# Kernel optimization log

Hardware: AMD Instinct MI355X
Metric: run time of the kernel (lower is better)

The kernel has to match this reference:

```python
import jax, jax.numpy as jnp
import numpy as np

# SemiConv2d with semifield_type='MaxMin':
#   out[n,oc,i,j] = max_{ic,kh,kw} min(x_pad[n,ic,i+kh,j+kw], kernel[oc,ic,kh,kw])
# stride=1, 'same' padding with -inf (identity of max).

def setup_inputs() -> dict:
    key = jax.random.key(0)
    kx, kk = jax.random.split(key)
    x = jax.random.normal(kx, (8, 32, 96, 96), dtype=jnp.float32)
    kernel = jax.random.normal(kk, (32, 32, 3, 3), dtype=jnp.float32)
    return {"x": x, "kernel": kernel}


def reference(x, kernel):
    N, IC, H, W = x.shape
    OC, IC2, KH, KW = kernel.shape
    assert IC == IC2
    # same padding for k=3, stride=1 (left=top=1, right=bottom=1)
    p = KH - 1
    top = left = p // 2
    bot = right = p - top
    xp = jnp.pad(x, ((0, 0), (0, 0), (top, bot), (left, right)),
                 constant_values=-jnp.inf)
    out = None
    # small fixed loop over kernel taps (KH*KW = 9); vectorized over N, OC, IC, H, W
    for kh in range(KH):
        for kw in range(KW):
            win = xp[:, :, kh:kh + H, kw:kw + W]           # [N, IC, H, W]
            k_tap = kernel[:, :, kh, kw]                   # [OC, IC]
            # min over values, max over input channels -> [N, OC, H, W]
            v = jnp.max(jnp.minimum(win[:, None], k_tap[None, :, :, None, None]), axis=2)
            out = v if out is None else jnp.maximum(out, v)
    return out
```

## Files before the change

kernel.cpp:

```cpp
#include <hip/hip_runtime.h>
#include <math.h>
#include <stdint.h>


#define HH 96
#define WW 96
#define CIN 32
#define OCN 32
#define XQ_ROWS 98
#define ROWB 200
#define SLICEB (XQ_ROWS * ROWB)
#define XQ_BYTES ((size_t)256 * SLICEB)
#define ROWU2 25
#define XQW_TOTAL (256 * XQ_ROWS * ROWU2)
#define XQWB (XQW_TOTAL / 256)
#define NROW 96
#define TBL_BYTES ((size_t)OCN * NROW * 16)
#define RMX_BYTES ((size_t)OCN * NROW * 4)
#define WS_NEED (XQ_BYTES + TBL_BYTES + RMX_BYTES)
#define NEGH2 0xFC00FC00u

typedef _Float16 h2 __attribute__((ext_vector_type(2)));
typedef uint32_t u2a4 __attribute__((ext_vector_type(2), aligned(4)));

__device__ __forceinline__ uint32_t pkmin_vs(uint32_t x, uint32_t k) {
    uint32_t d;
    asm("v_pk_min_f16 %0, %1, %2" : "=v"(d) : "v"(x), "s"(k));
    return d;
}
__device__ __forceinline__ uint32_t pkmin_vv(uint32_t a, uint32_t b) {
    uint32_t d;
    asm("v_pk_min_f16 %0, %1, %2" : "=v"(d) : "v"(a), "v"(b));
    return d;
}
__device__ __forceinline__ uint32_t pkmax(uint32_t a, uint32_t b) {
    uint32_t d;
    asm("v_pk_max_f16 %0, %1, %2" : "=v"(d) : "v"(a), "v"(b));
    return d;
}
__device__ __forceinline__ uint32_t packh2(float lo, float hi) {
    h2 p = {(_Float16)lo, (_Float16)hi};
    return __builtin_bit_cast(uint32_t, p);
}

__global__ __launch_bounds__(256) void setup_all(const float* __restrict__ x,
                                                 const float* __restrict__ kk,
                                                 uint2* __restrict__ xq,
                                                 uint4* __restrict__ tbl,
                                                 uint32_t* __restrict__ rmx) {
    __shared__ float rs[NROW];
    const int bb = blockIdx.x;
    if (bb < XQWB) {
        int idx = bb * 256 + threadIdx.x;
        int j8 = idx % ROWU2;
        int t  = idx / ROWU2;
        int hp = t % XQ_ROWS;
        int s  = t / XQ_ROWS;
        int h  = hp - 1;
        bool hv = (h >= 0) && (h < HH);
        const float* row = x + ((size_t)s * HH + (hv ? h : 0)) * WW;
        float v[4];
#pragma unroll
        for (int q = 0; q < 4; ++q) {
            int w = 4 * j8 - 1 + q;
            v[q] = (hv && w >= 0 && w < WW) ? row[w] : -INFINITY;
        }
        uint2 o;
        o.x = packh2(v[0], v[1]);
        o.y = packh2(v[2], v[3]);
        xq[idx] = o;
        return;
    }
    const int oc = bb - XQWB;
    const int t  = threadIdx.x;
    if (t >= NROW) return;
    const int ic = t / 3, dh = t - 3 * ic;
    const float* kp = kk + ((size_t)(oc * CIN + ic) * 3 + dh) * 3;
    float k0 = kp[0], k1 = kp[1], k2 = kp[2];
    float rm = fmaxf(fmaxf(k0, k1), k2);
    rs[t] = rm;
    __syncthreads();
    int rank = 0;
    for (int s = 0; s < NROW; ++s) {
        float v = rs[s];
        rank += (v > rm) || (v == rm && s < t);
    }
    uint32_t off = (uint32_t)(ic * XQ_ROWS + dh) * ROWB;
    tbl[oc * NROW + rank] = make_uint4(packh2(k0, k0), packh2(k1, k1),
                                       packh2(k2, k2), off);
    rmx[oc * NROW + rank] = packh2(rm, rm);
}

__global__ __launch_bounds__(192, 8) void semiconv_c(const char* __restrict__ xqb,
                                                     const uint4* __restrict__ tbl,
                                                     const uint32_t* __restrict__ rmx,
                                                     float* __restrict__ out) {
    const int tid = threadIdx.x;
    const int jj = tid % 48;
    const int hr = tid / 48;
    const int b  = blockIdx.x;
    const int n  = b & 7;
    const int t  = b >> 3;
    const int oc = t & 31;
    const int hp = t >> 5;
    const int h  = hp * 4 + hr;

    const char* xqn = xqb + (size_t)n * CIN * SLICEB;
    const int vbyte = h * ROWB + 4 * jj;
    const uint4* tb = tbl + oc * NROW;
    const uint32_t* rb = rmx + oc * NROW;

    uint32_t acc = NEGH2;

    for (int c = 0; c < NROW / 4; ++c) {
        uint4 e0 = tb[4 * c], e1 = tb[4 * c + 1], e2 = tb[4 * c + 2], e3 = tb[4 * c + 3];
        uint32_t kn = (c < NROW / 4 - 1) ? rb[4 * c + 4] : 0u;

        const char* r0 = xqn + e0.w;
        const char* r1 = xqn + e1.w;
        const char* r2 = xqn + e2.w;
        const char* r3 = xqn + e3.w;
        u2a4 q0 = *(const u2a4*)(r0 + vbyte);
        u2a4 q1 = *(const u2a4*)(r1 + vbyte);
        u2a4 q2 = *(const u2a4*)(r2 + vbyte);
        u2a4 q3 = *(const u2a4*)(r3 + vbyte);
        uint32_t v0 = __builtin_amdgcn_alignbit(q0.y, q0.x, 16);
        uint32_t v1 = __builtin_amdgcn_alignbit(q1.y, q1.x, 16);
        uint32_t v2 = __builtin_amdgcn_alignbit(q2.y, q2.x, 16);
        uint32_t v3 = __builtin_amdgcn_alignbit(q3.y, q3.x, 16);
        uint32_t m0 = pkmax(pkmax(pkmin_vs(q0.x, e0.x), pkmin_vs(v0, e0.y)),
                            pkmin_vs(q0.y, e0.z));
        uint32_t m1 = pkmax(pkmax(pkmin_vs(q1.x, e1.x), pkmin_vs(v1, e1.y)),
                            pkmin_vs(q1.y, e1.z));
        uint32_t m2 = pkmax(pkmax(pkmin_vs(q2.x, e2.x), pkmin_vs(v2, e2.y)),
                            pkmin_vs(q2.y, e2.z));
        uint32_t m3 = pkmax(pkmax(pkmin_vs(q3.x, e3.x), pkmin_vs(v3, e3.y)),
                            pkmin_vs(q3.y, e3.z));
        acc = pkmax(acc, pkmax(pkmax(m0, m1), pkmax(m2, m3)));

        if (c < NROW / 4 - 1) {
            uint32_t sw = __builtin_amdgcn_alignbit(acc, acc, 16);
            uint32_t mn = pkmin_vv(acc, sw);
            h2 a  = __builtin_bit_cast(h2, mn);
            h2 kv = __builtin_bit_cast(h2, kn);
            if (__all(a.x >= kv.x)) break;
        }
    }

    h2 a = __builtin_bit_cast(h2, acc);
    float2 v = make_float2((float)a.x, (float)a.y);
    *(float2*)(out + (((size_t)(n * OCN + oc)) * HH + h) * WW + 2 * jj) = v;
}

#define NEGINF (-INFINITY)
__global__ __launch_bounds__(192, 8) void semiconv2d_f32(
    const float* __restrict__ x, const float* __restrict__ kk, float* __restrict__ out)
{
    const int tid = threadIdx.x;
    const int w  = tid % WW;
    const int hr = tid / WW;
    const int b   = blockIdx.x;
    const int ocb = b & 7;
    const int hp  = (b >> 3) % 48;
    const int n   = (b >> 3) / 48;
    const int h   = hp * 2 + hr;
    const int oc0 = ocb * 4;
    float a0[4], a1[4], a2[4];
#pragma unroll
    for (int i = 0; i < 4; ++i) { a0[i] = NEGINF; a1[i] = NEGINF; a2[i] = NEGINF; }
    const bool vm = (h > 0), vp = (h < HH - 1);
    const int hm  = vm ? h - 1 : h;
    const int hpl = vp ? h + 1 : h;
    const int cm  = (w > 0) ? -1 : 0;
    const int cp  = (w < WW - 1) ? 1 : 0;
    const float* rm = x + ((size_t)(n * CIN) * HH + hm)  * WW + w;
    const float* r1 = x + ((size_t)(n * CIN) * HH + h)   * WW + w;
    const float* rp = x + ((size_t)(n * CIN) * HH + hpl) * WW + w;
#pragma unroll 2
    for (int ic = 0; ic < CIN; ++ic) {
        float r00 = vm ? rm[cm] : NEGINF, r01 = vm ? rm[0] : NEGINF, r02 = vm ? rm[cp] : NEGINF;
        float r10 = r1[cm], r11 = r1[0], r12 = r1[cp];
        float r20 = vp ? rp[cm] : NEGINF, r21 = vp ? rp[0] : NEGINF, r22 = vp ? rp[cp] : NEGINF;
#pragma unroll
        for (int oc = 0; oc < 4; ++oc) {
            const float* kq = kk + (size_t)(((oc0 + oc) * CIN + ic)) * 9;
            a0[oc] = fmaxf(fmaxf(a0[oc], fminf(r00, kq[0])), fmaxf(fminf(r10, kq[3]), fminf(r20, kq[6])));
            a1[oc] = fmaxf(fmaxf(a1[oc], fminf(r01, kq[1])), fmaxf(fminf(r11, kq[4]), fminf(r21, kq[7])));
            a2[oc] = fmaxf(fmaxf(a2[oc], fminf(r02, kq[2])), fmaxf(fminf(r12, kq[5]), fminf(r22, kq[8])));
        }
        rm += HH * WW; r1 += HH * WW; rp += HH * WW;
    }
#pragma unroll
    for (int oc = 0; oc < 4; ++oc) {
        float v0 = (w > 0)      ? a0[oc] : NEGINF;
        float v2 = (w < WW - 1) ? a2[oc] : NEGINF;
        out[(((size_t)(n * OCN + oc0 + oc)) * HH + h) * WW + w] = fmaxf(fmaxf(v0, a1[oc]), v2);
    }
}

extern "C" void kernel_launch(void* const* d_in, const int* in_sizes, int n_in,
                              void* d_out, int out_size, void* d_ws, size_t ws_size,
                              hipStream_t stream) {
    const float* x  = (const float*)d_in[0];
    const float* kk = (const float*)d_in[1];
    float* out      = (float*)d_out;
    if (ws_size >= WS_NEED) {
        uint2*    xq  = (uint2*)d_ws;
        uint4*    tbl = (uint4*)((char*)d_ws + XQ_BYTES);
        uint32_t* rmx = (uint32_t*)((char*)d_ws + XQ_BYTES + TBL_BYTES);
        setup_all<<<dim3(XQWB + OCN), dim3(256), 0, stream>>>(x, kk, xq, tbl, rmx);
        semiconv_c<<<dim3(8 * OCN * 24), dim3(192), 0, stream>>>(
            (const char*)xq, tbl, rmx, out);
    } else {
        semiconv2d_f32<<<dim3(8 * 48 * 8), dim3(192), 0, stream>>>(x, kk, out);
    }
}
```

Baseline: 91.31 us.

## Compute eight outputs per thread with 16-byte row loads and 208-byte rows

Each thread now produces eight adjacent output columns instead of two. It loads a 16-byte vector plus one extra dword per tap row and forms the shifted pairs with alignbit, so neighbouring outputs share the loaded data. The packed fp16 rows are padded to 208 bytes so the vector loads stay aligned, and output stores become two float4 writes. Blocks now cover 16 rows each, cutting load instructions per output. The early-exit test now needs all four accumulators across the wave, so a block may run more taps before it stops, and each thread holds more registers.

```diff
diff --git a/kernel.cpp b/kernel.cpp
--- a/kernel.cpp
+++ b/kernel.cpp
@@ -8,12 +8,12 @@
 #define CIN 32
 #define OCN 32
 #define XQ_ROWS 98
-#define ROWB 200
+#define ROWB 208
 #define SLICEB (XQ_ROWS * ROWB)
 #define XQ_BYTES ((size_t)256 * SLICEB)
-#define ROWU2 25
-#define XQW_TOTAL (256 * XQ_ROWS * ROWU2)
-#define XQWB (XQW_TOTAL / 256)
+#define ROWU4 13
+#define XQP_TOTAL (256 * XQ_ROWS * ROWU4)
+#define XQPB (XQP_TOTAL / 256)
 #define NROW 96
 #define TBL_BYTES ((size_t)OCN * NROW * 16)
 #define RMX_BYTES ((size_t)OCN * NROW * 4)
@@ -21,7 +21,6 @@
 #define NEGH2 0xFC00FC00u
 
 typedef _Float16 h2 __attribute__((ext_vector_type(2)));
-typedef uint32_t u2a4 __attribute__((ext_vector_type(2), aligned(4)));
 
 __device__ __forceinline__ uint32_t pkmin_vs(uint32_t x, uint32_t k) {
     uint32_t d;
@@ -45,33 +44,35 @@
 
 __global__ __launch_bounds__(256) void setup_all(const float* __restrict__ x,
                                                  const float* __restrict__ kk,
-                                                 uint2* __restrict__ xq,
+                                                 uint4* __restrict__ xq,
                                                  uint4* __restrict__ tbl,
                                                  uint32_t* __restrict__ rmx) {
     __shared__ float rs[NROW];
     const int bb = blockIdx.x;
-    if (bb < XQWB) {
+    if (bb < XQPB) {
         int idx = bb * 256 + threadIdx.x;
-        int j8 = idx % ROWU2;
-        int t  = idx / ROWU2;
+        int u  = idx % ROWU4;
+        int t  = idx / ROWU4;
         int hp = t % XQ_ROWS;
         int s  = t / XQ_ROWS;
         int h  = hp - 1;
         bool hv = (h >= 0) && (h < HH);
         const float* row = x + ((size_t)s * HH + (hv ? h : 0)) * WW;
-        float v[4];
-#pragma unroll
-        for (int q = 0; q < 4; ++q) {
-            int w = 4 * j8 - 1 + q;
+        float v[8];
+#pragma unroll
+        for (int q = 0; q < 8; ++q) {
+            int w = 8 * u - 1 + q;
             v[q] = (hv && w >= 0 && w < WW) ? row[w] : -INFINITY;
         }
-        uint2 o;
+        uint4 o;
         o.x = packh2(v[0], v[1]);
         o.y = packh2(v[2], v[3]);
+        o.z = packh2(v[4], v[5]);
+        o.w = packh2(v[6], v[7]);
         xq[idx] = o;
         return;
     }
-    const int oc = bb - XQWB;
+    const int oc = bb - XQPB;
     const int t  = threadIdx.x;
     if (t >= NROW) return;
     const int ic = t / 3, dh = t - 3 * ic;
@@ -91,65 +92,81 @@
     rmx[oc * NROW + rank] = packh2(rm, rm);
 }
 
-__global__ __launch_bounds__(192, 8) void semiconv_c(const char* __restrict__ xqb,
+__global__ __launch_bounds__(192, 8) void semiconv_w(const char* __restrict__ xqb,
                                                      const uint4* __restrict__ tbl,
                                                      const uint32_t* __restrict__ rmx,
                                                      float* __restrict__ out) {
     const int tid = threadIdx.x;
-    const int jj = tid % 48;
-    const int hr = tid / 48;
+    const int wl = tid % 12;
+    const int hh = tid / 12;
     const int b  = blockIdx.x;
-    const int n  = b & 7;
-    const int t  = b >> 3;
-    const int oc = t & 31;
-    const int hp = t >> 5;
-    const int h  = hp * 4 + hr;
+    const int oc = b & 31;
+    const int r  = b >> 5;
+    const int hq = r % 6;
+    const int n  = r / 6;
+    const int h  = hq * 16 + hh;
 
     const char* xqn = xqb + (size_t)n * CIN * SLICEB;
-    const int vbyte = h * ROWB + 4 * jj;
+    const int vb = h * ROWB + 16 * wl;
     const uint4* tb = tbl + oc * NROW;
     const uint32_t* rb = rmx + oc * NROW;
 
-    uint32_t acc = NEGH2;
-
-    for (int c = 0; c < NROW / 4; ++c) {
-        uint4 e0 = tb[4 * c], e1 = tb[4 * c + 1], e2 = tb[4 * c + 2], e3 = tb[4 * c + 3];
-        uint32_t kn = (c < NROW / 4 - 1) ? rb[4 * c + 4] : 0u;
+    uint32_t a0 = NEGH2, a1 = NEGH2, a2 = NEGH2, a3 = NEGH2;
+
+    for (int c = 0; c < NROW / 2; ++c) {
+        uint4 e0 = tb[2 * c], e1 = tb[2 * c + 1];
+        uint32_t kn = (c < NROW / 2 - 1) ? rb[2 * c + 2] : 0u;
 
         const char* r0 = xqn + e0.w;
         const char* r1 = xqn + e1.w;
-        const char* r2 = xqn + e2.w;
-        const char* r3 = xqn + e3.w;
-        u2a4 q0 = *(const u2a4*)(r0 + vbyte);
-        u2a4 q1 = *(const u2a4*)(r1 + vbyte);
-        u2a4 q2 = *(const u2a4*)(r2 + vbyte);
-        u2a4 q3 = *(const u2a4*)(r3 + vbyte);
-        uint32_t v0 = __builtin_amdgcn_alignbit(q0.y, q0.x, 16);
-        uint32_t v1 = __builtin_amdgcn_alignbit(q1.y, q1.x, 16);
-        uint32_t v2 = __builtin_amdgcn_alignbit(q2.y, q2.x, 16);
-        uint32_t v3 = __builtin_amdgcn_alignbit(q3.y, q3.x, 16);
-        uint32_t m0 = pkmax(pkmax(pkmin_vs(q0.x, e0.x), pkmin_vs(v0, e0.y)),
-                            pkmin_vs(q0.y, e0.z));
-        uint32_t m1 = pkmax(pkmax(pkmin_vs(q1.x, e1.x), pkmin_vs(v1, e1.y)),
-                            pkmin_vs(q1.y, e1.z));
-        uint32_t m2 = pkmax(pkmax(pkmin_vs(q2.x, e2.x), pkmin_vs(v2, e2.y)),
-                            pkmin_vs(q2.y, e2.z));
-        uint32_t m3 = pkmax(pkmax(pkmin_vs(q3.x, e3.x), pkmin_vs(v3, e3.y)),
-                            pkmin_vs(q3.y, e3.z));
-        acc = pkmax(acc, pkmax(pkmax(m0, m1), pkmax(m2, m3)));
-
-        if (c < NROW / 4 - 1) {
-            uint32_t sw = __builtin_amdgcn_alignbit(acc, acc, 16);
-            uint32_t mn = pkmin_vv(acc, sw);
+        uint4    d  = *(const uint4*)(r0 + vb);
+        uint32_t d4 = *(const uint32_t*)(r0 + vb + 16);
+        uint4    D  = *(const uint4*)(r1 + vb);
+        uint32_t D4 = *(const uint32_t*)(r1 + vb + 16);
+
+        uint32_t p01 = __builtin_amdgcn_alignbit(d.y, d.x, 16);
+        uint32_t p12 = __builtin_amdgcn_alignbit(d.z, d.y, 16);
+        uint32_t p23 = __builtin_amdgcn_alignbit(d.w, d.z, 16);
+        uint32_t p34 = __builtin_amdgcn_alignbit(d4,  d.w, 16);
+        a0 = pkmax(a0, pkmax(pkmax(pkmin_vs(d.x, e0.x), pkmin_vs(p01, e0.y)),
+                             pkmin_vs(d.y, e0.z)));
+        a1 = pkmax(a1, pkmax(pkmax(pkmin_vs(d.y, e0.x), pkmin_vs(p12, e0.y)),
+                             pkmin_vs(d.z, e0.z)));
+        a2 = pkmax(a2, pkmax(pkmax(pkmin_vs(d.z, e0.x), pkmin_vs(p23, e0.y)),
+                             pkmin_vs(d.w, e0.z)));
+        a3 = pkmax(a3, pkmax(pkmax(pkmin_vs(d.w, e0.x), pkmin_vs(p34, e0.y)),
+                             pkmin_vs(d4,  e0.z)));
+        uint32_t q01 = __builtin_amdgcn_alignbit(D.y, D.x, 16);
+        uint32_t q12 = __builtin_amdgcn_alignbit(D.z, D.y, 16);
+        uint32_t q23 = __builtin_amdgcn_alignbit(D.w, D.z, 16);
+        uint32_t q34 = __builtin_amdgcn_alignbit(D4,  D.w, 16);
+        a0 = pkmax(a0, pkmax(pkmax(pkmin_vs(D.x, e1.x), pkmin_vs(q01, e1.y)),
+                             pkmin_vs(D.y, e1.z)));
+        a1 = pkmax(a1, pkmax(pkmax(pkmin_vs(D.y, e1.x), pkmin_vs(q12, e1.y)),
+                             pkmin_vs(D.z, e1.z)));
+        a2 = pkmax(a2, pkmax(pkmax(pkmin_vs(D.z, e1.x), pkmin_vs(q23, e1.y)),
+                             pkmin_vs(D.w, e1.z)));
+        a3 = pkmax(a3, pkmax(pkmax(pkmin_vs(D.w, e1.x), pkmin_vs(q34, e1.y)),
+                             pkmin_vs(D4,  e1.z)));
+
+        if (c < NROW / 2 - 1) {
+            uint32_t mn = pkmin_vv(pkmin_vv(a0, a1), pkmin_vv(a2, a3));
+            mn = pkmin_vv(mn, __builtin_amdgcn_alignbit(mn, mn, 16));
             h2 a  = __builtin_bit_cast(h2, mn);
             h2 kv = __builtin_bit_cast(h2, kn);
             if (__all(a.x >= kv.x)) break;
         }
     }
 
-    h2 a = __builtin_bit_cast(h2, acc);
-    float2 v = make_float2((float)a.x, (float)a.y);
-    *(float2*)(out + (((size_t)(n * OCN + oc)) * HH + h) * WW + 2 * jj) = v;
+    float* ob = out + (((size_t)(n * OCN + oc)) * HH + h) * WW + 8 * wl;
+    h2 r0 = __builtin_bit_cast(h2, a0);
+    h2 r1 = __builtin_bit_cast(h2, a1);
+    h2 r2 = __builtin_bit_cast(h2, a2);
+    h2 r3 = __builtin_bit_cast(h2, a3);
+    float4 o1 = make_float4((float)r0.x, (float)r0.y, (float)r1.x, (float)r1.y);
+    float4 o2 = make_float4((float)r2.x, (float)r2.y, (float)r3.x, (float)r3.y);
+    *(float4*)(ob)     = o1;
+    *(float4*)(ob + 4) = o2;
 }
 
 #define NEGINF (-INFINITY)
@@ -205,11 +222,11 @@
     const float* kk = (const float*)d_in[1];
     float* out      = (float*)d_out;
     if (ws_size >= WS_NEED) {
-        uint2*    xq  = (uint2*)d_ws;
+        uint4*    xq  = (uint4*)d_ws;
         uint4*    tbl = (uint4*)((char*)d_ws + XQ_BYTES);
         uint32_t* rmx = (uint32_t*)((char*)d_ws + XQ_BYTES + TBL_BYTES);
-        setup_all<<<dim3(XQWB + OCN), dim3(256), 0, stream>>>(x, kk, xq, tbl, rmx);
-        semiconv_c<<<dim3(8 * OCN * 24), dim3(192), 0, stream>>>(
+        setup_all<<<dim3(XQPB + OCN), dim3(256), 0, stream>>>(x, kk, xq, tbl, rmx);
+        semiconv_w<<<dim3(8 * OCN * 6), dim3(192), 0, stream>>>(
             (const char*)xq, tbl, rmx, out);
     } else {
         semiconv2d_f32<<<dim3(8 * 48 * 8), dim3(192), 0, stream>>>(x, kk, out);
```

Result: faster. 88.16 us (-3.4%).
